# Performance work log

Measured on AMD Instinct MI355X. Metric: run time of the kernel, lower is better.

Reference implementation:

```python
import jax, jax.numpy as jnp
import numpy as np


def setup_inputs() -> dict:
    key = jax.random.key(0)
    ks = jax.random.split(key, 8)
    B, N = 4, 256
    E, C, H = 64, 128, 256
    return {
        "edge_features": jax.random.normal(ks[0], (B, E, N, N), dtype=jnp.float32),
        "node_features": jax.random.normal(ks[1], (B, C, N), dtype=jnp.float32),
        "W1": jax.random.normal(ks[2], (H, E + 2 * C), dtype=jnp.float32) * 0.05,
        "b1": jax.random.normal(ks[3], (H,), dtype=jnp.float32) * 0.05,
        "W2": jax.random.normal(ks[4], (H, H), dtype=jnp.float32) * 0.05,
        "b2": jax.random.normal(ks[5], (H,), dtype=jnp.float32) * 0.05,
        "W3": jax.random.normal(ks[6], (1, H), dtype=jnp.float32) * 0.05,
        "b3": jax.random.normal(ks[7], (1,), dtype=jnp.float32) * 0.05,
    }


def reference(edge_features, node_features, W1, b1, W2, b2, W3, b3):
    B, C, N = node_features.shape
    # node_addon_row: [B, C, N, N] broadcast along last dim; col along dim 2
    row = jnp.broadcast_to(node_features[:, :, :, None], (B, C, N, N))
    col = jnp.broadcast_to(node_features[:, :, None, :], (B, C, N, N))
    x = jnp.concatenate([edge_features, row, col], axis=1)  # [B, E+2C, N, N]
    # 1x1 conv == channel matmul
    x = jax.nn.relu(jnp.einsum('bcnm,oc->bonm', x, W1) + b1[None, :, None, None])
    x = jax.nn.relu(jnp.einsum('bcnm,oc->bonm', x, W2) + b2[None, :, None, None])
    x = jnp.einsum('bcnm,oc->bonm', x, W3) + b3[None, :, None, None]  # [B,1,N,N]
    return x[:, 0, :, :]
```

## Files before the change

### kernel.cpp

```cpp
#include <hip/hip_runtime.h>
#include <stdint.h>

typedef __bf16 bf16x8 __attribute__((ext_vector_type(8)));
typedef __bf16 bf16x4v __attribute__((ext_vector_type(4)));
typedef float  f32x16 __attribute__((ext_vector_type(16)));
typedef float  f32x4t __attribute__((ext_vector_type(4)));
typedef unsigned int u32x2 __attribute__((ext_vector_type(2)));

#define WS_W1S 0
#define WS_W2S 32768
#define WS_R   163840
#define WS_CT  1212416

__global__ void prep_weights(const float* __restrict__ W1, const float* __restrict__ W2,
                             __bf16* __restrict__ w1s, __bf16* __restrict__ w2s) {
    int t = blockIdx.x * 256 + threadIdx.x;
    int chunk = t >> 6, lane = t & 63;
    if (chunk < 128) {
        int wid = chunk >> 5, ks = (chunk >> 1) & 15, mb = chunk & 1;
        int o = wid * 64 + mb * 32 + (lane & 31);
        int k = ks * 16 + (lane >> 5) * 8;
        const float* src = W2 + o * 256 + k;
        __bf16* dst = w2s + chunk * 512 + lane * 8;
#pragma unroll
        for (int j = 0; j < 8; ++j) dst[j] = (__bf16)src[j];
    } else if (chunk < 160) {
        int c1 = chunk - 128;
        int wid = c1 >> 3, ks = (c1 >> 1) & 3, mb = c1 & 1;
        int o = wid * 64 + mb * 32 + (lane & 31);
        int k = ks * 16 + (lane >> 5) * 8;
        const float* src = W1 + o * 320 + k;
        __bf16* dst = w1s + c1 * 512 + lane * 8;
#pragma unroll
        for (int j = 0; j < 8; ++j) dst[j] = (__bf16)src[j];
    }
}

__global__ __launch_bounds__(256) void prep_rc(
    const float* __restrict__ W1, const float* __restrict__ b1,
    const float* __restrict__ node, float* __restrict__ Rt,
    __bf16* __restrict__ Ctb) {
    __shared__ float nds[128 * 16];
    const int b = blockIdx.x >> 4, j0 = (blockIdx.x & 15) * 16;
    const int o = threadIdx.x;
    {
        int c = threadIdx.x >> 1, jh = (threadIdx.x & 1) * 8;
        const float* src = node + b * 32768 + c * 256 + j0 + jh;
        *(float4*)&nds[c * 16 + jh] = *(const float4*)src;
        *(float4*)&nds[c * 16 + jh + 4] = *(const float4*)(src + 4);
    }
    __syncthreads();
    float aR[16], aC[16];
#pragma unroll
    for (int j = 0; j < 16; ++j) { aR[j] = 0.f; aC[j] = 0.f; }
    const float* wr = W1 + o * 320 + 64;
    const float* wc = W1 + o * 320 + 192;
    for (int c4 = 0; c4 < 32; ++c4) {
        float4 wrv = *(const float4*)(wr + c4 * 4);
        float4 wcv = *(const float4*)(wc + c4 * 4);
        const float* wrp = (const float*)&wrv;
        const float* wcp = (const float*)&wcv;
#pragma unroll
        for (int r = 0; r < 4; ++r) {
            const f32x4t* nrow = (const f32x4t*)&nds[(c4 * 4 + r) * 16];
            f32x4t n0 = nrow[0], n1 = nrow[1], n2 = nrow[2], n3 = nrow[3];
#pragma unroll
            for (int q = 0; q < 4; ++q) {
                aR[q]      = fmaf(wrp[r], n0[q], aR[q]);
                aR[q + 4]  = fmaf(wrp[r], n1[q], aR[q + 4]);
                aR[q + 8]  = fmaf(wrp[r], n2[q], aR[q + 8]);
                aR[q + 12] = fmaf(wrp[r], n3[q], aR[q + 12]);
                aC[q]      = fmaf(wcp[r], n0[q], aC[q]);
                aC[q + 4]  = fmaf(wcp[r], n1[q], aC[q + 4]);
                aC[q + 8]  = fmaf(wcp[r], n2[q], aC[q + 8]);
                aC[q + 12] = fmaf(wcp[r], n3[q], aC[q + 12]);
            }
        }
    }
    float bb = b1[o];
#pragma unroll
    for (int j = 0; j < 16; ++j) {
        int idx = ((b * 256 + j0 + j) << 8) + o;
        Rt[idx] = aR[j] + bb;
        Ctb[idx] = (__bf16)aC[j];
    }
}

__device__ inline void zero_acc(f32x16 acc[2][2]) {
#pragma unroll
    for (int i = 0; i < 2; ++i)
#pragma unroll
        for (int j = 0; j < 2; ++j)
#pragma unroll
            for (int k = 0; k < 16; ++k) acc[i][j][k] = 0.f;
}

__global__ __launch_bounds__(256, 2) void fused_main(
    const float* __restrict__ edge, const __bf16* __restrict__ w1s,
    const __bf16* __restrict__ w2s, const float* __restrict__ Rt,
    const __bf16* __restrict__ Ctb, const float* __restrict__ b2,
    const float* __restrict__ W3, const float* __restrict__ b3,
    float* __restrict__ out) {
    __shared__ unsigned int lds_e[64 * 33];
    __shared__ unsigned int lds_h1[64 * 140];
    __shared__ float lds_p[64 * 9];
    __shared__ float lds_c[512];

    const int tid = threadIdx.x;
    const int wid = tid >> 6;
    const int lane = tid & 63;
    const int p31 = lane & 31;
    const int hi = lane >> 5;
    const int obase = wid * 64;

    const int blk = blockIdx.x;
    const int b   = blk >> 7;
    const int m0  = ((blk >> 5) & 3) << 6;
    const int n0  = (blk & 31) << 3;

    lds_c[tid] = b2[tid];
    lds_c[256 + tid] = W3[tid];

    const float4* eg = (const float4*)edge;
    const int a_ = tid & 15;
    const int epb = tid >> 4;
    float4 pf[4];

#define PREFETCH(nn)                                                        \
    {                                                                       \
        _Pragma("unroll")                                                   \
        for (int r = 0; r < 2; ++r) {                                       \
            int ep = r * 16 + epb;                                          \
            int f4 = (b * 64 + ep * 2) * 16384 + (nn) * 64 + (m0 >> 2) + a_;\
            pf[r * 2]     = eg[f4];                                         \
            pf[r * 2 + 1] = eg[f4 + 16384];                                 \
        }                                                                   \
    }

#define LOAD_Q(bf, q)                                                       \
    {                                                                       \
        _Pragma("unroll")                                                   \
        for (int ksl = 0; ksl < 4; ++ksl)                                   \
            _Pragma("unroll")                                               \
            for (int mb = 0; mb < 2; ++mb)                                  \
                A2q[bf][ksl][mb] = *(const bf16x8*)(w2_s +                  \
                    ((((wid << 4) + (q) * 4 + ksl) << 1) + mb) * 512 + (lane << 3)); \
    }

    PREFETCH(n0);

    bf16x4v CvR[8][2];
#pragma unroll
    for (int mb = 0; mb < 2; ++mb)
#pragma unroll
        for (int rg = 0; rg < 4; ++rg)
#pragma unroll
            for (int nb = 0; nb < 2; ++nb)
                CvR[mb * 4 + rg][nb] = *(const bf16x4v*)(Ctb +
                    ((b * 256 + m0 + nb * 32 + p31) << 8) + obase + mb * 32 + 8 * rg + 4 * hi);

    f32x16 acc[2][2];
    bf16x8 A2q[2][4][2];
    for (int it = 0; it < 8; ++it) {
        const int n = n0 + it;

        uint64_t w1a = (uint64_t)w1s;
        asm volatile("" : "+s"(w1a));
        const __bf16* w1_s = (const __bf16*)w1a;
        uint64_t w2a = (uint64_t)w2s;
        asm volatile("" : "+s"(w2a));
        const __bf16* w2_s = (const __bf16*)w2a;

#pragma unroll
        for (int r = 0; r < 2; ++r) {
            int ep = r * 16 + epb;
            const float* p0 = (const float*)&pf[r * 2];
            const float* p1 = (const float*)&pf[r * 2 + 1];
#pragma unroll
            for (int i = 0; i < 4; ++i) {
                union { __bf16 h[2]; unsigned int u; } t;
                t.h[0] = (__bf16)p0[i];
                t.h[1] = (__bf16)p1[i];
                lds_e[(a_ * 4 + i) * 33 + ep] = t.u;
            }
        }
        bf16x8 A1[2][4];
#pragma unroll
        for (int mb = 0; mb < 2; ++mb)
#pragma unroll
            for (int ks = 0; ks < 4; ++ks)
                A1[mb][ks] = *(const bf16x8*)(w1_s +
                    ((((wid << 2) + ks) << 1) + mb) * 512 + (lane << 3));
        __syncthreads();

        zero_acc(acc);
#pragma unroll
        for (int ks = 0; ks < 4; ++ks) {
            bf16x8 B1[2];
#pragma unroll
            for (int nb = 0; nb < 2; ++nb) {
                union { unsigned int u[4]; bf16x8 v; } bb;
#pragma unroll
                for (int j = 0; j < 4; ++j)
                    bb.u[j] = lds_e[(nb * 32 + p31) * 33 + ks * 8 + hi * 4 + j];
                B1[nb] = bb.v;
            }
#pragma unroll
            for (int mb = 0; mb < 2; ++mb) {
                acc[mb][0] = __builtin_amdgcn_mfma_f32_32x32x16_bf16(A1[mb][ks], B1[0], acc[mb][0], 0, 0, 0);
                acc[mb][1] = __builtin_amdgcn_mfma_f32_32x32x16_bf16(A1[mb][ks], B1[1], acc[mb][1], 0, 0, 0);
            }
        }

        const int nRow = (b * 256 + n) << 8;
#pragma unroll
        for (int mb = 0; mb < 2; ++mb) {
#pragma unroll
            for (int rg = 0; rg < 4; ++rg) {
                int och = obase + mb * 32 + 8 * rg + 4 * hi;
                f32x4t Rv = *(const f32x4t*)(Rt + nRow + och);
#pragma unroll
                for (int nb = 0; nb < 2; ++nb) {
                    int pix = nb * 32 + p31;
                    bf16x4v Cv = CvR[mb * 4 + rg][nb];
                    union { __bf16 h[4]; u32x2 u; } t;
#pragma unroll
                    for (int rr = 0; rr < 4; ++rr) {
                        float v = acc[mb][nb][rg * 4 + rr] + Rv[rr] + (float)Cv[rr];
                        t.h[rr] = (__bf16)fmaxf(v, 0.f);
                    }
                    *(u32x2*)&lds_h1[pix * 140 + (och >> 1)] = t.u;
                }
            }
        }
        LOAD_Q(0, 0);
        if (it < 7) PREFETCH(n + 1);
        __syncthreads();

        zero_acc(acc);
#pragma unroll
        for (int q = 0; q < 4; ++q) {
            if (q < 3) LOAD_Q((q + 1) & 1, q + 1);
#pragma unroll
            for (int ksl = 0; ksl < 4; ++ksl) {
                const int ksg = q * 4 + ksl;
                bf16x8 B2[2];
#pragma unroll
                for (int nb = 0; nb < 2; ++nb)
                    B2[nb] = *(const bf16x8*)&lds_h1[(nb * 32 + p31) * 140 + ksg * 8 + hi * 4];
#pragma unroll
                for (int mb = 0; mb < 2; ++mb) {
                    acc[mb][0] = __builtin_amdgcn_mfma_f32_32x32x16_bf16(A2q[q & 1][ksl][mb], B2[0], acc[mb][0], 0, 0, 0);
                    acc[mb][1] = __builtin_amdgcn_mfma_f32_32x32x16_bf16(A2q[q & 1][ksl][mb], B2[1], acc[mb][1], 0, 0, 0);
                }
            }
        }

        float part0 = 0.f, part1 = 0.f;
#pragma unroll
        for (int mb = 0; mb < 2; ++mb) {
#pragma unroll
            for (int rg = 0; rg < 4; ++rg) {
                int och = obase + mb * 32 + 8 * rg + 4 * hi;
                f32x4t b2v = *(const f32x4t*)&lds_c[och];
                f32x4t w3v = *(const f32x4t*)&lds_c[256 + och];
#pragma unroll
                for (int rr = 0; rr < 4; ++rr) {
                    float h0 = fmaxf(acc[mb][0][rg * 4 + rr] + b2v[rr], 0.f);
                    float h1v = fmaxf(acc[mb][1][rg * 4 + rr] + b2v[rr], 0.f);
                    part0 = fmaf(w3v[rr], h0, part0);
                    part1 = fmaf(w3v[rr], h1v, part1);
                }
            }
        }
        lds_p[(0 * 32 + p31) * 9 + wid * 2 + hi] = part0;
        lds_p[(1 * 32 + p31) * 9 + wid * 2 + hi] = part1;
        __syncthreads();

        if (tid < 64) {
            float s = b3[0];
#pragma unroll
            for (int k = 0; k < 8; ++k) s += lds_p[tid * 9 + k];
            out[((b * 256 + n) << 8) + m0 + tid] = s;
        }
    }
#undef PREFETCH
#undef LOAD_Q
}

extern "C" void kernel_launch(void* const* d_in, const int* in_sizes, int n_in,
                              void* d_out, int out_size, void* d_ws, size_t ws_size,
                              hipStream_t stream) {
    const float* edge = (const float*)d_in[0];
    const float* node = (const float*)d_in[1];
    const float* W1   = (const float*)d_in[2];
    const float* b1   = (const float*)d_in[3];
    const float* W2   = (const float*)d_in[4];
    const float* b2   = (const float*)d_in[5];
    const float* W3   = (const float*)d_in[6];
    const float* b3   = (const float*)d_in[7];
    char* ws = (char*)d_ws;
    __bf16* w1s = (__bf16*)(ws + WS_W1S);
    __bf16* w2s = (__bf16*)(ws + WS_W2S);
    float*  Rt  = (float*)(ws + WS_R);
    __bf16* Ctb = (__bf16*)(ws + WS_CT);

    prep_weights<<<40, 256, 0, stream>>>(W1, W2, w1s, w2s);
    prep_rc<<<64, 256, 0, stream>>>(W1, b1, node, Rt, Ctb);
    fused_main<<<512, 256, 0, stream>>>(edge, w1s, w2s, Rt, Ctb, b2, W3, b3, (float*)d_out);
}
```

Before: 160.2 us.

## Process two rows per layer-2 GEMM with swizzled H1 LDS and pre-swizzled C table

The main loop now runs layer 1 for two consecutive n rows and stacks both into a 128-pixel H1 tile in LDS. Layer 2 then runs as one wider GEMM, so each W2 fragment loaded from global memory feeds twice as many MFMAs. The H1 tile uses an XOR-swizzled layout instead of padding, and the column-contribution table is stored pre-swizzled so each lane can load it contiguously. In exchange, LDS use roughly doubles (about 64KB for H1) and accumulator register pressure grows, which may limit occupancy below the requested two blocks per CU.

```diff
diff --git a/kernel.cpp b/kernel.cpp
--- a/kernel.cpp
+++ b/kernel.cpp
@@ -39,7 +39,7 @@
 __global__ __launch_bounds__(256) void prep_rc(
     const float* __restrict__ W1, const float* __restrict__ b1,
     const float* __restrict__ node, float* __restrict__ Rt,
-    __bf16* __restrict__ Ctb) {
+    __bf16* __restrict__ Cts) {
     __shared__ float nds[128 * 16];
     const int b = blockIdx.x >> 4, j0 = (blockIdx.x & 15) * 16;
     const int o = threadIdx.x;
@@ -78,33 +78,29 @@
         }
     }
     float bb = b1[o];
+    const int wid = o >> 6, mb = (o >> 5) & 1, rg = (o >> 3) & 3;
+    const int hi = (o >> 2) & 1, oq = o & 3;
 #pragma unroll
     for (int j = 0; j < 16; ++j) {
-        int idx = ((b * 256 + j0 + j) << 8) + o;
-        Rt[idx] = aR[j] + bb;
-        Ctb[idx] = (__bf16)aC[j];
-    }
-}
-
-__device__ inline void zero_acc(f32x16 acc[2][2]) {
-#pragma unroll
-    for (int i = 0; i < 2; ++i)
-#pragma unroll
-        for (int j = 0; j < 2; ++j)
-#pragma unroll
-            for (int k = 0; k < 16; ++k) acc[i][j][k] = 0.f;
+        int m = j0 + j;
+        Rt[((b * 256 + m) << 8) + o] = aR[j] + bb;
+        int mg = m >> 6, nbm = (m >> 5) & 1, p31m = m & 31;
+        int chunk = ((((b * 4 + mg) * 4 + wid) * 2 + mb) * 4 + rg) * 2 + nbm;
+        Cts[chunk * 256 + (hi * 32 + p31m) * 4 + oq] = (__bf16)aC[j];
+    }
 }
 
 __global__ __launch_bounds__(256, 2) void fused_main(
     const float* __restrict__ edge, const __bf16* __restrict__ w1s,
     const __bf16* __restrict__ w2s, const float* __restrict__ Rt,
-    const __bf16* __restrict__ Ctb, const float* __restrict__ b2,
+    const __bf16* __restrict__ Cts, const float* __restrict__ b2,
     const float* __restrict__ W3, const float* __restrict__ b3,
     float* __restrict__ out) {
     __shared__ unsigned int lds_e[64 * 33];
-    __shared__ unsigned int lds_h1[64 * 140];
-    __shared__ float lds_p[64 * 9];
+    __shared__ unsigned int lds_h1[128 * 128];
+    __shared__ float lds_p[128 * 9];
     __shared__ float lds_c[512];
+    char* h1b = (char*)lds_h1;
 
     const int tid = threadIdx.x;
     const int wid = tid >> 6;
@@ -115,7 +111,8 @@
 
     const int blk = blockIdx.x;
     const int b   = blk >> 7;
-    const int m0  = ((blk >> 5) & 3) << 6;
+    const int mg  = (blk >> 5) & 3;
+    const int m0  = mg << 6;
     const int n0  = (blk & 31) << 3;
 
     lds_c[tid] = b2[tid];
@@ -137,32 +134,104 @@
         }                                                                   \
     }
 
-#define LOAD_Q(bf, q)                                                       \
-    {                                                                       \
-        _Pragma("unroll")                                                   \
-        for (int ksl = 0; ksl < 4; ++ksl)                                   \
+#define STAGE_E()                                                           \
+    {                                                                       \
+        _Pragma("unroll")                                                   \
+        for (int r = 0; r < 2; ++r) {                                       \
+            int ep = r * 16 + epb;                                          \
+            const float* p0 = (const float*)&pf[r * 2];                     \
+            const float* p1 = (const float*)&pf[r * 2 + 1];                 \
+            _Pragma("unroll")                                               \
+            for (int i = 0; i < 4; ++i) {                                   \
+                union { __bf16 h[2]; unsigned int u; } t;                   \
+                t.h[0] = (__bf16)p0[i];                                     \
+                t.h[1] = (__bf16)p1[i];                                     \
+                lds_e[(a_ * 4 + i) * 33 + ep] = t.u;                        \
+            }                                                               \
+        }                                                                   \
+    }
+
+#define LOADSUB(bf, s)                                                      \
+    {                                                                       \
+        _Pragma("unroll")                                                   \
+        for (int ksl = 0; ksl < 2; ++ksl)                                   \
             _Pragma("unroll")                                               \
             for (int mb = 0; mb < 2; ++mb)                                  \
-                A2q[bf][ksl][mb] = *(const bf16x8*)(w2_s +                  \
-                    ((((wid << 4) + (q) * 4 + ksl) << 1) + mb) * 512 + (lane << 3)); \
+                A2s[bf][ksl][mb] = *(const bf16x8*)(w2_s +                  \
+                    ((((wid << 4) + (s) * 2 + ksl) << 1) + mb) * 512 + (lane << 3)); \
+    }
+
+#define LAYER1()                                                            \
+    {                                                                       \
+        _Pragma("unroll")                                                   \
+        for (int mb = 0; mb < 2; ++mb)                                      \
+            _Pragma("unroll")                                               \
+            for (int nbm = 0; nbm < 2; ++nbm)                               \
+                _Pragma("unroll")                                           \
+                for (int k = 0; k < 16; ++k) acc[mb][nbm][k] = 0.f;         \
+        _Pragma("unroll")                                                   \
+        for (int ks = 0; ks < 4; ++ks) {                                    \
+            bf16x8 B1[2];                                                   \
+            _Pragma("unroll")                                               \
+            for (int nbm = 0; nbm < 2; ++nbm) {                             \
+                union { unsigned int u[4]; bf16x8 v; } bb;                  \
+                _Pragma("unroll")                                           \
+                for (int j = 0; j < 4; ++j)                                 \
+                    bb.u[j] = lds_e[(nbm * 32 + p31) * 33 + ks * 8 + hi * 4 + j]; \
+                B1[nbm] = bb.v;                                             \
+            }                                                               \
+            _Pragma("unroll")                                               \
+            for (int mb = 0; mb < 2; ++mb) {                                \
+                acc[mb][0] = __builtin_amdgcn_mfma_f32_32x32x16_bf16(A1[mb][ks], B1[0], acc[mb][0], 0, 0, 0); \
+                acc[mb][1] = __builtin_amdgcn_mfma_f32_32x32x16_bf16(A1[mb][ks], B1[1], acc[mb][1], 0, 0, 0); \
+            }                                                               \
+        }                                                                   \
+    }
+
+#define EPI1(R, nn)                                                         \
+    {                                                                       \
+        const int nRow = (b * 256 + (nn)) << 8;                             \
+        _Pragma("unroll")                                                   \
+        for (int mb = 0; mb < 2; ++mb) {                                    \
+            _Pragma("unroll")                                               \
+            for (int rg = 0; rg < 4; ++rg) {                                \
+                int och = obase + mb * 32 + 8 * rg + 4 * hi;                \
+                f32x4t Rv = *(const f32x4t*)(Rt + nRow + och);              \
+                int col16 = (wid << 3) + (mb << 2) + rg;                    \
+                _Pragma("unroll")                                           \
+                for (int nbm = 0; nbm < 2; ++nbm) {                         \
+                    int p = (R) * 64 + nbm * 32 + p31;                      \
+                    bf16x4v Cv = CvR[(mb * 4 + rg) * 2 + nbm];              \
+                    union { __bf16 h[4]; u32x2 u; } t;                      \
+                    _Pragma("unroll")                                       \
+                    for (int rr = 0; rr < 4; ++rr) {                        \
+                        float v = acc[mb][nbm][rg * 4 + rr] + Rv[rr] + (float)Cv[rr]; \
+                        t.h[rr] = (__bf16)fmaxf(v, 0.f);                    \
+                    }                                                       \
+                    *(u32x2*)(h1b + p * 512 + ((col16 ^ p31) << 4) + (hi << 3)) = t.u; \
+                }                                                           \
+            }                                                               \
+        }                                                                   \
     }
 
     PREFETCH(n0);
 
-    bf16x4v CvR[8][2];
+    bf16x4v CvR[16];
 #pragma unroll
     for (int mb = 0; mb < 2; ++mb)
 #pragma unroll
         for (int rg = 0; rg < 4; ++rg)
 #pragma unroll
-            for (int nb = 0; nb < 2; ++nb)
-                CvR[mb * 4 + rg][nb] = *(const bf16x4v*)(Ctb +
-                    ((b * 256 + m0 + nb * 32 + p31) << 8) + obase + mb * 32 + 8 * rg + 4 * hi);
-
-    f32x16 acc[2][2];
-    bf16x8 A2q[2][4][2];
-    for (int it = 0; it < 8; ++it) {
-        const int n = n0 + it;
+            for (int nbm = 0; nbm < 2; ++nbm) {
+                int chunk = ((((b * 4 + mg) * 4 + wid) * 2 + mb) * 4 + rg) * 2 + nbm;
+                CvR[(mb * 4 + rg) * 2 + nbm] = *(const bf16x4v*)(Cts + chunk * 256 + lane * 4);
+            }
+
+    f32x16 acc[2][4];
+    bf16x8 A2s[2][2][2];
+#pragma unroll 1
+    for (int it = 0; it < 4; ++it) {
+        const int n = n0 + it * 2;
 
         uint64_t w1a = (uint64_t)w1s;
         asm volatile("" : "+s"(w1a));
@@ -171,19 +240,7 @@
         asm volatile("" : "+s"(w2a));
         const __bf16* w2_s = (const __bf16*)w2a;
 
-#pragma unroll
-        for (int r = 0; r < 2; ++r) {
-            int ep = r * 16 + epb;
-            const float* p0 = (const float*)&pf[r * 2];
-            const float* p1 = (const float*)&pf[r * 2 + 1];
-#pragma unroll
-            for (int i = 0; i < 4; ++i) {
-                union { __bf16 h[2]; unsigned int u; } t;
-                t.h[0] = (__bf16)p0[i];
-                t.h[1] = (__bf16)p1[i];
-                lds_e[(a_ * 4 + i) * 33 + ep] = t.u;
-            }
-        }
+        STAGE_E();
         bf16x8 A1[2][4];
 #pragma unroll
         for (int mb = 0; mb < 2; ++mb)
@@ -193,70 +250,49 @@
                     ((((wid << 2) + ks) << 1) + mb) * 512 + (lane << 3));
         __syncthreads();
 
-        zero_acc(acc);
-#pragma unroll
-        for (int ks = 0; ks < 4; ++ks) {
-            bf16x8 B1[2];
-#pragma unroll
-            for (int nb = 0; nb < 2; ++nb) {
-                union { unsigned int u[4]; bf16x8 v; } bb;
-#pragma unroll
-                for (int j = 0; j < 4; ++j)
-                    bb.u[j] = lds_e[(nb * 32 + p31) * 33 + ks * 8 + hi * 4 + j];
-                B1[nb] = bb.v;
-            }
-#pragma unroll
-            for (int mb = 0; mb < 2; ++mb) {
-                acc[mb][0] = __builtin_amdgcn_mfma_f32_32x32x16_bf16(A1[mb][ks], B1[0], acc[mb][0], 0, 0, 0);
-                acc[mb][1] = __builtin_amdgcn_mfma_f32_32x32x16_bf16(A1[mb][ks], B1[1], acc[mb][1], 0, 0, 0);
+        PREFETCH(n + 1);
+        LAYER1();
+        EPI1(0, n);
+        __syncthreads();
+
+        STAGE_E();
+        __syncthreads();
+
+        if (it < 3) PREFETCH(n + 2);
+        LAYER1();
+        EPI1(1, n + 1);
+        __syncthreads();
+
+#pragma unroll
+        for (int mb = 0; mb < 2; ++mb)
+#pragma unroll
+            for (int nb = 0; nb < 4; ++nb)
+#pragma unroll
+                for (int k = 0; k < 16; ++k) acc[mb][nb][k] = 0.f;
+        LOADSUB(0, 0);
+#pragma unroll
+        for (int s = 0; s < 8; ++s) {
+            if (s < 7) LOADSUB((s + 1) & 1, s + 1);
+#pragma unroll
+            for (int ksl = 0; ksl < 2; ++ksl) {
+                const int ksg = s * 2 + ksl;
+                bf16x8 B2[4];
+#pragma unroll
+                for (int nb = 0; nb < 4; ++nb) {
+                    int p = nb * 32 + p31;
+                    B2[nb] = *(const bf16x8*)(h1b + p * 512 +
+                             ((((ksg << 1) + hi) ^ p31) << 4));
+                }
+#pragma unroll
+                for (int mb = 0; mb < 2; ++mb)
+#pragma unroll
+                    for (int nb = 0; nb < 4; ++nb)
+                        acc[mb][nb] = __builtin_amdgcn_mfma_f32_32x32x16_bf16(
+                            A2s[s & 1][ksl][mb], B2[nb], acc[mb][nb], 0, 0, 0);
             }
         }
 
-        const int nRow = (b * 256 + n) << 8;
-#pragma unroll
-        for (int mb = 0; mb < 2; ++mb) {
-#pragma unroll
-            for (int rg = 0; rg < 4; ++rg) {
-                int och = obase + mb * 32 + 8 * rg + 4 * hi;
-                f32x4t Rv = *(const f32x4t*)(Rt + nRow + och);
-#pragma unroll
-                for (int nb = 0; nb < 2; ++nb) {
-                    int pix = nb * 32 + p31;
-                    bf16x4v Cv = CvR[mb * 4 + rg][nb];
-                    union { __bf16 h[4]; u32x2 u; } t;
-#pragma unroll
-                    for (int rr = 0; rr < 4; ++rr) {
-                        float v = acc[mb][nb][rg * 4 + rr] + Rv[rr] + (float)Cv[rr];
-                        t.h[rr] = (__bf16)fmaxf(v, 0.f);
-                    }
-                    *(u32x2*)&lds_h1[pix * 140 + (och >> 1)] = t.u;
-                }
-            }
-        }
-        LOAD_Q(0, 0);
-        if (it < 7) PREFETCH(n + 1);
-        __syncthreads();
-
-        zero_acc(acc);
-#pragma unroll
-        for (int q = 0; q < 4; ++q) {
-            if (q < 3) LOAD_Q((q + 1) & 1, q + 1);
-#pragma unroll
-            for (int ksl = 0; ksl < 4; ++ksl) {
-                const int ksg = q * 4 + ksl;
-                bf16x8 B2[2];
-#pragma unroll
-                for (int nb = 0; nb < 2; ++nb)
-                    B2[nb] = *(const bf16x8*)&lds_h1[(nb * 32 + p31) * 140 + ksg * 8 + hi * 4];
-#pragma unroll
-                for (int mb = 0; mb < 2; ++mb) {
-                    acc[mb][0] = __builtin_amdgcn_mfma_f32_32x32x16_bf16(A2q[q & 1][ksl][mb], B2[0], acc[mb][0], 0, 0, 0);
-                    acc[mb][1] = __builtin_amdgcn_mfma_f32_32x32x16_bf16(A2q[q & 1][ksl][mb], B2[1], acc[mb][1], 0, 0, 0);
-                }
-            }
-        }
-
-        float part0 = 0.f, part1 = 0.f;
+        float part[4] = {0.f, 0.f, 0.f, 0.f};
 #pragma unroll
         for (int mb = 0; mb < 2; ++mb) {
 #pragma unroll
@@ -266,26 +302,31 @@
                 f32x4t w3v = *(const f32x4t*)&lds_c[256 + och];
 #pragma unroll
                 for (int rr = 0; rr < 4; ++rr) {
-                    float h0 = fmaxf(acc[mb][0][rg * 4 + rr] + b2v[rr], 0.f);
-                    float h1v = fmaxf(acc[mb][1][rg * 4 + rr] + b2v[rr], 0.f);
-                    part0 = fmaf(w3v[rr], h0, part0);
-                    part1 = fmaf(w3v[rr], h1v, part1);
+#pragma unroll
+                    for (int nb = 0; nb < 4; ++nb) {
+                        float h = fmaxf(acc[mb][nb][rg * 4 + rr] + b2v[rr], 0.f);
+                        part[nb] = fmaf(w3v[rr], h, part[nb]);
+                    }
                 }
             }
         }
-        lds_p[(0 * 32 + p31) * 9 + wid * 2 + hi] = part0;
-        lds_p[(1 * 32 + p31) * 9 + wid * 2 + hi] = part1;
-        __syncthreads();
-
-        if (tid < 64) {
+#pragma unroll
+        for (int nb = 0; nb < 4; ++nb)
+            lds_p[(nb * 32 + p31) * 9 + wid * 2 + hi] = part[nb];
+        __syncthreads();
+
+        if (tid < 128) {
             float s = b3[0];
 #pragma unroll
             for (int k = 0; k < 8; ++k) s += lds_p[tid * 9 + k];
-            out[((b * 256 + n) << 8) + m0 + tid] = s;
+            out[((b * 256 + n + (tid >> 6)) << 8) + m0 + (tid & 63)] = s;
         }
     }
 #undef PREFETCH
-#undef LOAD_Q
+#undef STAGE_E
+#undef LOADSUB
+#undef LAYER1
+#undef EPI1
 }
 
 extern "C" void kernel_launch(void* const* d_in, const int* in_sizes, int n_in,
@@ -303,9 +344,9 @@
     __bf16* w1s = (__bf16*)(ws + WS_W1S);
     __bf16* w2s = (__bf16*)(ws + WS_W2S);
     float*  Rt  = (float*)(ws + WS_R);
-    __bf16* Ctb = (__bf16*)(ws + WS_CT);
+    __bf16* Cts = (__bf16*)(ws + WS_CT);
 
     prep_weights<<<40, 256, 0, stream>>>(W1, W2, w1s, w2s);
-    prep_rc<<<64, 256, 0, stream>>>(W1, b1, node, Rt, Ctb);
-    fused_main<<<512, 256, 0, stream>>>(edge, w1s, w2s, Rt, Ctb, b2, W3, b3, (float*)d_out);
+    prep_rc<<<64, 256, 0, stream>>>(W1, b1, node, Rt, Cts);
+    fused_main<<<512, 256, 0, stream>>>(edge, w1s, w2s, Rt, Cts, b2, W3, b3, (float*)d_out);
 }
```

Measured after the change: 208.7 us. 1.3x slower.
